# Kernel optimization log

Measured on AMD Instinct MI355X. Metric: run time of the kernel, lower is better.

## Reference

```python
import jax, jax.numpy as jnp
import numpy as np

TEMPERATURE = 0.1
NORMALIZED = True


def _l2norm(x, eps=1e-12):
    # matches F.normalize(p=2, dim=1)
    n = jnp.sqrt(jnp.sum(x * x, axis=1, keepdims=True))
    return x / jnp.maximum(n, eps)


def setup_inputs() -> dict:
    key = jax.random.key(0)
    k1, k2, k3, k4 = jax.random.split(key, 4)
    B, D = 4096, 256
    return {
        "hs": jax.random.normal(k1, (B, D), dtype=jnp.float32),
        "ht0": jax.random.normal(k2, (B, D), dtype=jnp.float32),
        "ht1": jax.random.normal(k3, (B, D), dtype=jnp.float32),
        "labels": jax.random.randint(k4, (B,), 0, 100, dtype=jnp.int64)
        if jax.config.jax_enable_x64 else jax.random.randint(k4, (B,), 0, 100, dtype=jnp.int32),
        "num_views": 2,
    }


def _per_teacher_loss(hs_n, ht_n, mask, logits_mask, batch_size, num_views):
    # features: [N, D] with N = 2B
    features = jnp.concatenate([hs_n, ht_n], axis=0)
    sim = jnp.matmul(features, features.T) / TEMPERATURE          # [N, N]
    exp_logits = jnp.exp(sim) * logits_mask                        # [N, N]
    log_prob = sim - jnp.log(jnp.sum(exp_logits, axis=1, keepdims=True))
    per_inst = -jnp.sum(mask * log_prob, axis=1) / jnp.sum(mask, axis=1)  # [N]
    if num_views > 1:
        per_inst = per_inst.reshape(batch_size, num_views).mean(axis=1)
    return per_inst.mean()


def reference(hs, ht0, ht1, labels, num_views):
    batch_size = labels.shape[0]
    hs = hs.reshape(batch_size, -1)
    ht_list = [ht0.reshape(batch_size, -1), ht1.reshape(batch_size, -1)]
    if NORMALIZED:
        hs = _l2norm(hs)
        ht_list = [_l2norm(ht) for ht in ht_list]

    labels2 = jnp.concatenate([labels, labels])                    # [N]
    mask = (labels2[:, None] == labels2[None, :]).astype(jnp.float32)
    N = 2 * batch_size
    logits_mask = 1.0 - jnp.eye(N, dtype=jnp.float32)              # zero diagonal
    mask = mask * logits_mask

    inter_loss = 0.0
    for ht in ht_list:
        inter_loss = inter_loss + _per_teacher_loss(
            hs, ht, mask, logits_mask, batch_size, num_views)
    return inter_loss / len(ht_list)
```

## Files before the change

### kernel.cpp

```cpp
#include <hip/hip_runtime.h>
#include <hip/hip_bf16.h>

#define B_SIZE 4096
#define D_SIZE 256
#define N_SIZE 8192
#define LOG2E10 14.4269504089f

#if __has_builtin(__builtin_amdgcn_exp2f)
#define FAST_EXP2(x) __builtin_amdgcn_exp2f(x)
#else
#define FAST_EXP2(x) __expf((x) * 0.69314718056f)
#endif

typedef __attribute__((ext_vector_type(8))) short short8;
typedef __attribute__((ext_vector_type(4))) short short4v;
typedef __attribute__((ext_vector_type(4))) float floatx4;


__device__ __forceinline__ void async16(void* lds, const void* g) {
    __builtin_amdgcn_global_load_lds(
        (const __attribute__((address_space(1))) unsigned int*)g,
        (__attribute__((address_space(3))) unsigned int*)lds, 16, 0, 0);
}

__device__ __forceinline__ void pair_from_q(int q, int& R, int& C) {
    int r = (int)((1.0f + sqrtf(1.0f + 8.0f * (float)q)) * 0.5f);
    while (r * (r - 1) / 2 > q) --r;
    while ((r + 1) * r / 2 <= q) ++r;
    R = r; C = q - r * (r - 1) / 2;
}

__global__ void norm_kernel(const float* __restrict__ hs,
                            const float* __restrict__ ht0,
                            const float* __restrict__ ht1,
                            __hip_bfloat16* __restrict__ dst,
                            float* __restrict__ zero_region,
                            const int* __restrict__ labels,
                            int* __restrict__ cnt, int* __restrict__ offv,
                            int* __restrict__ idxS) {
    const int tid = threadIdx.x;
    const int wv  = tid >> 6;
    const int l   = tid & 63;
    const int gid = blockIdx.x * 256 + tid;
    if (gid < 16386) zero_region[gid] = 0.0f;

    const int row = blockIdx.x * 4 + wv;
    const float* src = (row < 4096) ? (hs + row * D_SIZE)
                     : (row < 8192) ? (ht0 + (row - 4096) * D_SIZE)
                                    : (ht1 + (row - 8192) * D_SIZE);
    floatx4 x = *reinterpret_cast<const floatx4*>(src + l * 4);
    float ss = x[0] * x[0] + x[1] * x[1] + x[2] * x[2] + x[3] * x[3];
#pragma unroll
    for (int off = 32; off > 0; off >>= 1) ss += __shfl_xor(ss, off);
    float inv = 1.0f / fmaxf(sqrtf(ss), 1e-12f);
    short4v o;
#pragma unroll
    for (int k = 0; k < 4; ++k) {
        __hip_bfloat16 h = __float2bfloat16(x[k] * inv);
        o[k] = *reinterpret_cast<short*>(&h);
    }
    *reinterpret_cast<short4v*>(dst + row * D_SIZE + l * 4) = o;

    if (blockIdx.x == 0) {
        __shared__ int h[128], o2[128], ctr[128];
        if (tid < 128) { h[tid] = 0; ctr[tid] = 0; }
        __syncthreads();
        for (int i = tid; i < B_SIZE; i += 256) atomicAdd(&h[labels[i] & 127], 1);
        __syncthreads();
        if (tid == 0) {
            int s = 0;
            for (int c = 0; c < 128; ++c) { o2[c] = s; s += h[c]; }
        }
        __syncthreads();
        for (int i = tid; i < B_SIZE; i += 256) {
            int lab = labels[i] & 127;
            int pos = o2[lab] + atomicAdd(&ctr[lab], 1);
            idxS[pos] = i;
        }
        if (tid < 128) { cnt[tid] = h[tid]; offv[tid] = o2[tid]; }
    }
}

__global__ void gvec_kernel(const __hip_bfloat16* __restrict__ featBase,
                            const int* __restrict__ cnt,
                            const int* __restrict__ off,
                            const int* __restrict__ idxS,
                            float* __restrict__ gOut) {
    const int c   = blockIdx.x & 127;
    const int set = blockIdx.x >> 7;
    const int tid = threadIdx.x;
    const __hip_bfloat16* f = featBase + set * B_SIZE * D_SIZE;
    __shared__ int sIdx[256];
    const int n = cnt[c], o = off[c];
    float acc = 0.0f;
    for (int base = 0; base < n; base += 256) {
        int m = n - base; if (m > 256) m = 256;
        __syncthreads();
        if (tid < m) sIdx[tid] = idxS[o + base + tid];
        __syncthreads();
        for (int k = 0; k < m; ++k)
            acc += __bfloat162float(f[sIdx[k] * D_SIZE + tid]);
    }
    gOut[set * 32768 + c * 256 + tid] = acc;
}

__global__ __launch_bounds__(256, 2)
void sim_kernel(const __hip_bfloat16* __restrict__ featS,
                const __hip_bfloat16* __restrict__ featT0,
                const __hip_bfloat16* __restrict__ featT1,
                float* __restrict__ Sarr) {
    __shared__ __align__(16) unsigned char sB[2][32768];

    const int tid  = threadIdx.x;
    const int w    = tid >> 6;
    const int l    = tid & 63;
    const int quad = l >> 4;
    const int lcol = l & 15;

    int itemR[3], itemC[3], itemT[3], ni;
    if (blockIdx.x < 480) {
        ni = 2;
#pragma unroll
        for (int k = 0; k < 2; ++k) {
            int m = blockIdx.x * 2 + k;
            pair_from_q(m >> 1, itemR[k], itemC[k]);
            itemT[k] = m & 1;
        }
    } else {
        ni = 3;
        int i = blockIdx.x - 480;
        int m = 960 + i;
        pair_from_q(m >> 1, itemR[0], itemC[0]);
        itemT[0] = m & 1;
        itemR[1] = itemC[1] = i; itemT[1] = 0;
        itemR[2] = itemC[2] = i; itemT[2] = 1;
    }

    for (int it = 0; it < ni; ++it) {
        const int R = itemR[it], C = itemC[it], t = itemT[it];
        const __hip_bfloat16* featT = t ? featT1 : featT0;
        const int row_base = R * 256 + w * 64;
        const int col0 = C * 256;

        short8 af[4][8];
#pragma unroll
        for (int rt = 0; rt < 4; ++rt) {
            int arow = row_base + rt * 16 + lcol;
            const __hip_bfloat16* ap = (arow < B_SIZE) ? featS + arow * D_SIZE
                                                       : featT + (arow - B_SIZE) * D_SIZE;
#pragma unroll
            for (int ks = 0; ks < 8; ++ks)
                af[rt][ks] = *reinterpret_cast<const short8*>(ap + ks * 32 + quad * 8);
        }

        float Sp[4][4];
#pragma unroll
        for (int rt = 0; rt < 4; ++rt)
#pragma unroll
            for (int r = 0; r < 4; ++r) Sp[rt][r] = 0.0f;

        auto stage = [&](int b, int cb) {
            int tb = cb + w * 16;
            const __hip_bfloat16* cp = (tb < B_SIZE) ? featS + tb * D_SIZE
                                                     : featT + (tb - B_SIZE) * D_SIZE;
            const char* gp = (const char*)cp + (l & 15) * 512 + (l >> 4) * 16;
            unsigned char* lp = &sB[b][w * 8192];
#pragma unroll
            for (int ks = 0; ks < 8; ++ks)
                async16(lp + ks * 1024, gp + ks * 64);
        };

        stage(0, col0);

        for (int g = 0; g < 4; ++g) {
            const int buf = g & 1;
            __syncthreads();
            if (g + 1 < 4) stage(buf ^ 1, col0 + (g + 1) * 64);

            const int gcol = col0 + g * 64;
            if (gcol > row_base) continue;
            const bool dg = (gcol == row_base);

            float Cp[4] = {0.f, 0.f, 0.f, 0.f};
#pragma unroll
            for (int up = 0; up < 2; ++up) {
                floatx4 acc[2][4];
#pragma unroll
                for (int j = 0; j < 2; ++j)
#pragma unroll
                    for (int rt = 0; rt < 4; ++rt) acc[j][rt] = floatx4{0.f, 0.f, 0.f, 0.f};

#pragma unroll
                for (int ks = 0; ks < 8; ++ks) {
                    short8 bf[2];
#pragma unroll
                    for (int j = 0; j < 2; ++j)
                        bf[j] = *reinterpret_cast<const short8*>(
                            &sB[buf][(up * 2 + j) * 8192 + ks * 1024 + l * 16]);
#pragma unroll
                    for (int j = 0; j < 2; ++j)
#pragma unroll
                        for (int rt = 0; rt < 4; ++rt)
                            acc[j][rt] = __builtin_amdgcn_mfma_f32_16x16x32_bf16(
                                af[rt][ks], bf[j], acc[j][rt], 0, 0, 0);
                }
#pragma unroll
                for (int j = 0; j < 2; ++j)
#pragma unroll
                    for (int rt = 0; rt < 4; ++rt)
#pragma unroll
                        for (int r = 0; r < 4; ++r) {
                            float e = FAST_EXP2(acc[j][rt][r] * LOG2E10);
                            Sp[rt][r] += e;
                            Cp[up * 2 + j] += e;
                        }
            }

            if (!dg) {
#pragma unroll
                for (int u = 0; u < 4; ++u) {
                    Cp[u] += __shfl_xor(Cp[u], 16);
                    Cp[u] += __shfl_xor(Cp[u], 32);
                }
                if (quad == 0) {
#pragma unroll
                    for (int u = 0; u < 4; ++u)
                        atomicAdd(&Sarr[t * N_SIZE + gcol + u * 16 + lcol], Cp[u]);
                }
            }
        }

#pragma unroll
        for (int rt = 0; rt < 4; ++rt)
#pragma unroll
            for (int r = 0; r < 4; ++r) {
#pragma unroll
                for (int m = 1; m < 16; m <<= 1) Sp[rt][r] += __shfl_xor(Sp[rt][r], m);
            }
        if (lcol == 0) {
#pragma unroll
            for (int rt = 0; rt < 4; ++rt)
#pragma unroll
                for (int r = 0; r < 4; ++r) {
                    int row = row_base + rt * 16 + quad * 4 + r;
                    atomicAdd(&Sarr[t * N_SIZE + row], Sp[rt][r]);
                }
        }
    }
}

__global__ void rowstat_kernel(const __hip_bfloat16* __restrict__ featS,
                               const __hip_bfloat16* __restrict__ featT0,
                               const __hip_bfloat16* __restrict__ featT1,
                               const int* __restrict__ labels,
                               const float* __restrict__ gAll,
                               const int* __restrict__ cnt,
                               const float* __restrict__ Sarr,
                               float* __restrict__ lossAcc,
                               int* __restrict__ ticket,
                               float* __restrict__ out) {
    __shared__ float wpart[4];
    const int tid = threadIdx.x;
    const int wv  = tid >> 6;
    const int l   = tid & 63;
    const int waveid = blockIdx.x * 4 + wv;
    float psum = 0.0f;

    for (int it = 0; it < 8; ++it) {
        int R = waveid * 8 + it;
        int t = R >> 13;
        int i = R & (N_SIZE - 1);
        const __hip_bfloat16* f = (i < B_SIZE) ? featS + i * D_SIZE
                                : (t ? featT1 : featT0) + (i - B_SIZE) * D_SIZE;
        int lab = labels[i & (B_SIZE - 1)] & 127;
        short4v fb = *reinterpret_cast<const short4v*>(f + l * 4);
        float fx[4];
#pragma unroll
        for (int k = 0; k < 4; ++k) {
            unsigned int u = ((unsigned int)(unsigned short)fb[k]) << 16;
            fx[k] = __uint_as_float(u);
        }
        const float* gS = gAll + lab * 256 + l * 4;
        const float* gT = gAll + (1 + t) * 32768 + lab * 256 + l * 4;
        float dot = 0.f, aii = 0.f;
#pragma unroll
        for (int k = 0; k < 4; ++k) {
            dot += fx[k] * (gS[k] + gT[k]);
            aii += fx[k] * fx[k];
        }
#pragma unroll
        for (int m = 1; m < 64; m <<= 1) {
            dot += __shfl_xor(dot, m);
            aii += __shfl_xor(aii, m);
        }
        if (l == 0) {
            float S = Sarr[t * N_SIZE + i];
            float M = 2.0f * (float)cnt[lab] - 1.0f;
            float E = FAST_EXP2(LOG2E10 * aii);
            psum += logf(S - E) - 10.0f * (dot - aii) / M;
        }
    }
    if (l == 0) wpart[wv] = psum;
    __syncthreads();
    if (tid == 0) {
        atomicAdd(lossAcc, wpart[0] + wpart[1] + wpart[2] + wpart[3]);
        __threadfence();
        if (atomicAdd(ticket, 1) == 511) {
            float tot = atomicAdd(lossAcc, 0.0f);
            out[0] = tot / 16384.0f;
        }
    }
}

extern "C" void kernel_launch(void* const* d_in, const int* in_sizes, int n_in,
                              void* d_out, int out_size, void* d_ws, size_t ws_size,
                              hipStream_t stream) {
    const float* hs     = (const float*)d_in[0];
    const float* ht0    = (const float*)d_in[1];
    const float* ht1    = (const float*)d_in[2];
    const int*   labels = (const int*)d_in[3];

    char* ws = (char*)d_ws;
    float* Sarr    = (float*)(ws);
    float* lossAcc = (float*)(ws + 65536);
    int*   ticket  = (int*)(ws + 65540);
    int*   cnt     = (int*)(ws + 66048);
    int*   offv    = (int*)(ws + 66560);
    int*   idxS    = (int*)(ws + 67072);
    float* gAll    = (float*)(ws + 83968);
    __hip_bfloat16* featS  = (__hip_bfloat16*)(ws + 524288);
    __hip_bfloat16* featT0 = (__hip_bfloat16*)(ws + 524288 + 2097152);
    __hip_bfloat16* featT1 = (__hip_bfloat16*)(ws + 524288 + 2 * 2097152);

    norm_kernel<<<3072, 256, 0, stream>>>(hs, ht0, ht1, featS, (float*)ws,
                                          labels, cnt, offv, idxS);
    gvec_kernel<<<384, 256, 0, stream>>>(featS, cnt, offv, idxS, gAll);
    sim_kernel<<<512, 256, 0, stream>>>(featS, featT0, featT1, Sarr);
    rowstat_kernel<<<512, 256, 0, stream>>>(featS, featT0, featT1, labels, gAll, cnt,
                                            Sarr, lossAcc, ticket, (float*)d_out);
}
```

Baseline: 176.2 us.

## Use 512-row by 256-col sim tiles with single-shot LDS staging

The similarity kernel now runs 512-thread blocks (8 waves), each covering 512 rows against a 256-column strip. Each block loads the whole 256-column B tile into four LDS buffers in one async pass, replacing the double-buffered per-group pipeline and the multi-item loop. The triangular tile mapping is recomputed for the new 2:1 tile shape, with a separate path for diagonal blocks. The goal is more reuse of each LDS B tile across rows and fewer barriers, at the cost of 128KB of LDS per block, which limits occupancy, and no overlap between loads and compute.

```diff
diff --git a/kernel.cpp b/kernel.cpp
--- a/kernel.cpp
+++ b/kernel.cpp
@@ -21,13 +21,6 @@
     __builtin_amdgcn_global_load_lds(
         (const __attribute__((address_space(1))) unsigned int*)g,
         (__attribute__((address_space(3))) unsigned int*)lds, 16, 0, 0);
-}
-
-__device__ __forceinline__ void pair_from_q(int q, int& R, int& C) {
-    int r = (int)((1.0f + sqrtf(1.0f + 8.0f * (float)q)) * 0.5f);
-    while (r * (r - 1) / 2 > q) --r;
-    while ((r + 1) * r / 2 <= q) ++r;
-    R = r; C = q - r * (r - 1) / 2;
 }
 
 __global__ void norm_kernel(const float* __restrict__ hs,
@@ -104,12 +97,12 @@
     gOut[set * 32768 + c * 256 + tid] = acc;
 }
 
-__global__ __launch_bounds__(256, 2)
+__global__ __launch_bounds__(512, 2)
 void sim_kernel(const __hip_bfloat16* __restrict__ featS,
                 const __hip_bfloat16* __restrict__ featT0,
                 const __hip_bfloat16* __restrict__ featT1,
                 float* __restrict__ Sarr) {
-    __shared__ __align__(16) unsigned char sB[2][32768];
+    __shared__ __align__(16) unsigned char sB[4][32768];
 
     const int tid  = threadIdx.x;
     const int w    = tid >> 6;
@@ -117,135 +110,130 @@
     const int quad = l >> 4;
     const int lcol = l & 15;
 
-    int itemR[3], itemC[3], itemT[3], ni;
+    int RB, C, t;
     if (blockIdx.x < 480) {
-        ni = 2;
-#pragma unroll
-        for (int k = 0; k < 2; ++k) {
-            int m = blockIdx.x * 2 + k;
-            pair_from_q(m >> 1, itemR[k], itemC[k]);
-            itemT[k] = m & 1;
-        }
+        t = blockIdx.x & 1;
+        int q = blockIdx.x >> 1;
+        int r = (int)((1.0f + sqrtf(1.0f + 4.0f * (float)q)) * 0.5f);
+        while (r * (r - 1) > q) --r;
+        while (r * (r + 1) <= q) ++r;
+        RB = r; C = q - r * (r - 1);
     } else {
-        ni = 3;
         int i = blockIdx.x - 480;
-        int m = 960 + i;
-        pair_from_q(m >> 1, itemR[0], itemC[0]);
-        itemT[0] = m & 1;
-        itemR[1] = itemC[1] = i; itemT[1] = 0;
-        itemR[2] = itemC[2] = i; itemT[2] = 1;
-    }
-
-    for (int it = 0; it < ni; ++it) {
-        const int R = itemR[it], C = itemC[it], t = itemT[it];
-        const __hip_bfloat16* featT = t ? featT1 : featT0;
-        const int row_base = R * 256 + w * 64;
-        const int col0 = C * 256;
-
-        short8 af[4][8];
-#pragma unroll
-        for (int rt = 0; rt < 4; ++rt) {
-            int arow = row_base + rt * 16 + lcol;
-            const __hip_bfloat16* ap = (arow < B_SIZE) ? featS + arow * D_SIZE
-                                                       : featT + (arow - B_SIZE) * D_SIZE;
-#pragma unroll
-            for (int ks = 0; ks < 8; ++ks)
-                af[rt][ks] = *reinterpret_cast<const short8*>(ap + ks * 32 + quad * 8);
-        }
-
-        float Sp[4][4];
+        t = i & 1;
+        int s = i >> 1;
+        RB = s >> 1;
+        C = (RB << 1) + (s & 1);
+    }
+
+    const __hip_bfloat16* featT = t ? featT1 : featT0;
+    const int row_base = RB * 512 + w * 64;
+    const int col0 = C * 256;
+
+    short8 af[4][8];
+#pragma unroll
+    for (int rt = 0; rt < 4; ++rt) {
+        int arow = row_base + rt * 16 + lcol;
+        const __hip_bfloat16* ap = (arow < B_SIZE) ? featS + arow * D_SIZE
+                                                   : featT + (arow - B_SIZE) * D_SIZE;
+#pragma unroll
+        for (int ks = 0; ks < 8; ++ks)
+            af[rt][ks] = *reinterpret_cast<const short8*>(ap + ks * 32 + quad * 8);
+    }
+
+    {
+        const int u   = w >> 1;
+        const int ks0 = (w & 1) * 4;
+        const int tb  = col0 + u * 16;
+        const __hip_bfloat16* cp = (tb < B_SIZE) ? featS + tb * D_SIZE
+                                                 : featT + (tb - B_SIZE) * D_SIZE;
+        const char* gp = (const char*)cp + (l & 15) * 512 + (l >> 4) * 16;
+#pragma unroll
+        for (int g = 0; g < 4; ++g)
+#pragma unroll
+            for (int kk = 0; kk < 4; ++kk) {
+                int ks = ks0 + kk;
+                async16(&sB[g][u * 8192 + ks * 1024], gp + g * 32768 + ks * 64);
+            }
+    }
+
+    float Sp[4][4];
+#pragma unroll
+    for (int rt = 0; rt < 4; ++rt)
+#pragma unroll
+        for (int r = 0; r < 4; ++r) Sp[rt][r] = 0.0f;
+
+    __syncthreads();
+
+    for (int g = 0; g < 4; ++g) {
+        const int gcol = col0 + g * 64;
+        if (gcol > row_base) continue;
+        const bool dg = (gcol == row_base);
+
+        float Cp[4] = {0.f, 0.f, 0.f, 0.f};
+#pragma unroll
+        for (int up = 0; up < 2; ++up) {
+            floatx4 acc[2][4];
+#pragma unroll
+            for (int j = 0; j < 2; ++j)
+#pragma unroll
+                for (int rt = 0; rt < 4; ++rt) acc[j][rt] = floatx4{0.f, 0.f, 0.f, 0.f};
+
+#pragma unroll
+            for (int ks = 0; ks < 8; ++ks) {
+                short8 bf[2];
+#pragma unroll
+                for (int j = 0; j < 2; ++j)
+                    bf[j] = *reinterpret_cast<const short8*>(
+                        &sB[g][(up * 2 + j) * 8192 + ks * 1024 + l * 16]);
+#pragma unroll
+                for (int j = 0; j < 2; ++j)
+#pragma unroll
+                    for (int rt = 0; rt < 4; ++rt)
+                        acc[j][rt] = __builtin_amdgcn_mfma_f32_16x16x32_bf16(
+                            af[rt][ks], bf[j], acc[j][rt], 0, 0, 0);
+            }
+#pragma unroll
+            for (int j = 0; j < 2; ++j)
+#pragma unroll
+                for (int rt = 0; rt < 4; ++rt)
+#pragma unroll
+                    for (int r = 0; r < 4; ++r) {
+                        float e = FAST_EXP2(acc[j][rt][r] * LOG2E10);
+                        Sp[rt][r] += e;
+                        Cp[up * 2 + j] += e;
+                    }
+        }
+
+        if (!dg) {
+#pragma unroll
+            for (int u = 0; u < 4; ++u) {
+                Cp[u] += __shfl_xor(Cp[u], 16);
+                Cp[u] += __shfl_xor(Cp[u], 32);
+            }
+            if (quad == 0) {
+#pragma unroll
+                for (int u = 0; u < 4; ++u)
+                    atomicAdd(&Sarr[t * N_SIZE + gcol + u * 16 + lcol], Cp[u]);
+            }
+        }
+    }
+
+#pragma unroll
+    for (int rt = 0; rt < 4; ++rt)
+#pragma unroll
+        for (int r = 0; r < 4; ++r) {
+#pragma unroll
+            for (int m = 1; m < 16; m <<= 1) Sp[rt][r] += __shfl_xor(Sp[rt][r], m);
+        }
+    if (lcol == 0) {
 #pragma unroll
         for (int rt = 0; rt < 4; ++rt)
 #pragma unroll
-            for (int r = 0; r < 4; ++r) Sp[rt][r] = 0.0f;
-
-        auto stage = [&](int b, int cb) {
-            int tb = cb + w * 16;
-            const __hip_bfloat16* cp = (tb < B_SIZE) ? featS + tb * D_SIZE
-                                                     : featT + (tb - B_SIZE) * D_SIZE;
-            const char* gp = (const char*)cp + (l & 15) * 512 + (l >> 4) * 16;
-            unsigned char* lp = &sB[b][w * 8192];
-#pragma unroll
-            for (int ks = 0; ks < 8; ++ks)
-                async16(lp + ks * 1024, gp + ks * 64);
-        };
-
-        stage(0, col0);
-
-        for (int g = 0; g < 4; ++g) {
-            const int buf = g & 1;
-            __syncthreads();
-            if (g + 1 < 4) stage(buf ^ 1, col0 + (g + 1) * 64);
-
-            const int gcol = col0 + g * 64;
-            if (gcol > row_base) continue;
-            const bool dg = (gcol == row_base);
-
-            float Cp[4] = {0.f, 0.f, 0.f, 0.f};
-#pragma unroll
-            for (int up = 0; up < 2; ++up) {
-                floatx4 acc[2][4];
-#pragma unroll
-                for (int j = 0; j < 2; ++j)
-#pragma unroll
-                    for (int rt = 0; rt < 4; ++rt) acc[j][rt] = floatx4{0.f, 0.f, 0.f, 0.f};
-
-#pragma unroll
-                for (int ks = 0; ks < 8; ++ks) {
-                    short8 bf[2];
-#pragma unroll
-                    for (int j = 0; j < 2; ++j)
-                        bf[j] = *reinterpret_cast<const short8*>(
-                            &sB[buf][(up * 2 + j) * 8192 + ks * 1024 + l * 16]);
-#pragma unroll
-                    for (int j = 0; j < 2; ++j)
-#pragma unroll
-                        for (int rt = 0; rt < 4; ++rt)
-                            acc[j][rt] = __builtin_amdgcn_mfma_f32_16x16x32_bf16(
-                                af[rt][ks], bf[j], acc[j][rt], 0, 0, 0);
-                }
-#pragma unroll
-                for (int j = 0; j < 2; ++j)
-#pragma unroll
-                    for (int rt = 0; rt < 4; ++rt)
-#pragma unroll
-                        for (int r = 0; r < 4; ++r) {
-                            float e = FAST_EXP2(acc[j][rt][r] * LOG2E10);
-                            Sp[rt][r] += e;
-                            Cp[up * 2 + j] += e;
-                        }
-            }
-
-            if (!dg) {
-#pragma unroll
-                for (int u = 0; u < 4; ++u) {
-                    Cp[u] += __shfl_xor(Cp[u], 16);
-                    Cp[u] += __shfl_xor(Cp[u], 32);
-                }
-                if (quad == 0) {
-#pragma unroll
-                    for (int u = 0; u < 4; ++u)
-                        atomicAdd(&Sarr[t * N_SIZE + gcol + u * 16 + lcol], Cp[u]);
-                }
-            }
-        }
-
-#pragma unroll
-        for (int rt = 0; rt < 4; ++rt)
-#pragma unroll
             for (int r = 0; r < 4; ++r) {
-#pragma unroll
-                for (int m = 1; m < 16; m <<= 1) Sp[rt][r] += __shfl_xor(Sp[rt][r], m);
-            }
-        if (lcol == 0) {
-#pragma unroll
-            for (int rt = 0; rt < 4; ++rt)
-#pragma unroll
-                for (int r = 0; r < 4; ++r) {
-                    int row = row_base + rt * 16 + quad * 4 + r;
-                    atomicAdd(&Sarr[t * N_SIZE + row], Sp[rt][r]);
-                }
-        }
+                int row = row_base + rt * 16 + quad * 4 + r;
+                atomicAdd(&Sarr[t * N_SIZE + row], Sp[rt][r]);
+            }
     }
 }
 
@@ -335,7 +323,7 @@
     norm_kernel<<<3072, 256, 0, stream>>>(hs, ht0, ht1, featS, (float*)ws,
                                           labels, cnt, offv, idxS);
     gvec_kernel<<<384, 256, 0, stream>>>(featS, cnt, offv, idxS, gAll);
-    sim_kernel<<<512, 256, 0, stream>>>(featS, featT0, featT1, Sarr);
+    sim_kernel<<<544, 512, 0, stream>>>(featS, featT0, featT1, Sarr);
     rowstat_kernel<<<512, 256, 0, stream>>>(featS, featT0, featT1, labels, gAll, cnt,
                                             Sarr, lossAcc, ticket, (float*)d_out);
 }
```

Result: no change. 177.0 us (+0.4%).

## Fuse label grouping and class sums into per-class loss kernel, simplify sim grid

Applied to the files above, without the earlier changes.

The label histogram and sort in the norm kernel, plus the separate gvec kernel, are removed. They are replaced by a classstat kernel that launches one block per class: each block gathers its member indices, builds the class feature sums in shared memory, and computes the per-instance loss terms. The sim kernel drops its hand-balanced 2-or-3 tiles per block and launches a 528x2 grid with one triangular tile per block, the diagonal now included in the pair indexing. This cuts one launch and the global gather buffers, but loses the sim load balancing. Per-class blocks also make the final loss stage uneven and only 128 blocks wide.

```diff
diff --git a/kernel.cpp b/kernel.cpp
--- a/kernel.cpp
+++ b/kernel.cpp
@@ -9,7 +9,7 @@
 #if __has_builtin(__builtin_amdgcn_exp2f)
 #define FAST_EXP2(x) __builtin_amdgcn_exp2f(x)
 #else
-#define FAST_EXP2(x) __expf((x) * 0.69314718056f)
+#define FAST_EXP2(x) exp2f(x)
 #endif
 
 typedef __attribute__((ext_vector_type(8))) short short8;
@@ -25,19 +25,16 @@
 
 __device__ __forceinline__ void pair_from_q(int q, int& R, int& C) {
     int r = (int)((1.0f + sqrtf(1.0f + 8.0f * (float)q)) * 0.5f);
-    while (r * (r - 1) / 2 > q) --r;
-    while ((r + 1) * r / 2 <= q) ++r;
-    R = r; C = q - r * (r - 1) / 2;
+    while (r * (r + 1) / 2 > q) --r;
+    while ((r + 1) * (r + 2) / 2 <= q) ++r;
+    R = r; C = q - r * (r + 1) / 2;
 }
 
 __global__ void norm_kernel(const float* __restrict__ hs,
                             const float* __restrict__ ht0,
                             const float* __restrict__ ht1,
                             __hip_bfloat16* __restrict__ dst,
-                            float* __restrict__ zero_region,
-                            const int* __restrict__ labels,
-                            int* __restrict__ cnt, int* __restrict__ offv,
-                            int* __restrict__ idxS) {
+                            float* __restrict__ zero_region) {
     const int tid = threadIdx.x;
     const int wv  = tid >> 6;
     const int l   = tid & 63;
@@ -60,48 +57,6 @@
         o[k] = *reinterpret_cast<short*>(&h);
     }
     *reinterpret_cast<short4v*>(dst + row * D_SIZE + l * 4) = o;
-
-    if (blockIdx.x == 0) {
-        __shared__ int h[128], o2[128], ctr[128];
-        if (tid < 128) { h[tid] = 0; ctr[tid] = 0; }
-        __syncthreads();
-        for (int i = tid; i < B_SIZE; i += 256) atomicAdd(&h[labels[i] & 127], 1);
-        __syncthreads();
-        if (tid == 0) {
-            int s = 0;
-            for (int c = 0; c < 128; ++c) { o2[c] = s; s += h[c]; }
-        }
-        __syncthreads();
-        for (int i = tid; i < B_SIZE; i += 256) {
-            int lab = labels[i] & 127;
-            int pos = o2[lab] + atomicAdd(&ctr[lab], 1);
-            idxS[pos] = i;
-        }
-        if (tid < 128) { cnt[tid] = h[tid]; offv[tid] = o2[tid]; }
-    }
-}
-
-__global__ void gvec_kernel(const __hip_bfloat16* __restrict__ featBase,
-                            const int* __restrict__ cnt,
-                            const int* __restrict__ off,
-                            const int* __restrict__ idxS,
-                            float* __restrict__ gOut) {
-    const int c   = blockIdx.x & 127;
-    const int set = blockIdx.x >> 7;
-    const int tid = threadIdx.x;
-    const __hip_bfloat16* f = featBase + set * B_SIZE * D_SIZE;
-    __shared__ int sIdx[256];
-    const int n = cnt[c], o = off[c];
-    float acc = 0.0f;
-    for (int base = 0; base < n; base += 256) {
-        int m = n - base; if (m > 256) m = 256;
-        __syncthreads();
-        if (tid < m) sIdx[tid] = idxS[o + base + tid];
-        __syncthreads();
-        for (int k = 0; k < m; ++k)
-            acc += __bfloat162float(f[sIdx[k] * D_SIZE + tid]);
-    }
-    gOut[set * 32768 + c * 256 + tid] = acc;
 }
 
 __global__ __launch_bounds__(256, 2)
@@ -111,182 +66,182 @@
                 float* __restrict__ Sarr) {
     __shared__ __align__(16) unsigned char sB[2][32768];
 
+    const int p = blockIdx.x;
+    const int t = blockIdx.y;
+    const __hip_bfloat16* featT = t ? featT1 : featT0;
+
+    int R, C;
+    pair_from_q(p, R, C);
+
     const int tid  = threadIdx.x;
     const int w    = tid >> 6;
     const int l    = tid & 63;
     const int quad = l >> 4;
     const int lcol = l & 15;
-
-    int itemR[3], itemC[3], itemT[3], ni;
-    if (blockIdx.x < 480) {
-        ni = 2;
-#pragma unroll
-        for (int k = 0; k < 2; ++k) {
-            int m = blockIdx.x * 2 + k;
-            pair_from_q(m >> 1, itemR[k], itemC[k]);
-            itemT[k] = m & 1;
-        }
-    } else {
-        ni = 3;
-        int i = blockIdx.x - 480;
-        int m = 960 + i;
-        pair_from_q(m >> 1, itemR[0], itemC[0]);
-        itemT[0] = m & 1;
-        itemR[1] = itemC[1] = i; itemT[1] = 0;
-        itemR[2] = itemC[2] = i; itemT[2] = 1;
-    }
-
-    for (int it = 0; it < ni; ++it) {
-        const int R = itemR[it], C = itemC[it], t = itemT[it];
-        const __hip_bfloat16* featT = t ? featT1 : featT0;
-        const int row_base = R * 256 + w * 64;
-        const int col0 = C * 256;
-
-        short8 af[4][8];
-#pragma unroll
-        for (int rt = 0; rt < 4; ++rt) {
-            int arow = row_base + rt * 16 + lcol;
-            const __hip_bfloat16* ap = (arow < B_SIZE) ? featS + arow * D_SIZE
-                                                       : featT + (arow - B_SIZE) * D_SIZE;
-#pragma unroll
-            for (int ks = 0; ks < 8; ++ks)
-                af[rt][ks] = *reinterpret_cast<const short8*>(ap + ks * 32 + quad * 8);
-        }
-
-        float Sp[4][4];
+    const int row_base = R * 256 + w * 64;
+
+    short8 af[4][8];
+#pragma unroll
+    for (int rt = 0; rt < 4; ++rt) {
+        int arow = row_base + rt * 16 + lcol;
+        const __hip_bfloat16* ap = (arow < B_SIZE) ? featS + arow * D_SIZE
+                                                   : featT + (arow - B_SIZE) * D_SIZE;
+#pragma unroll
+        for (int ks = 0; ks < 8; ++ks)
+            af[rt][ks] = *reinterpret_cast<const short8*>(ap + ks * 32 + quad * 8);
+    }
+
+    float Sp[4][4];
+#pragma unroll
+    for (int rt = 0; rt < 4; ++rt)
+#pragma unroll
+        for (int r = 0; r < 4; ++r) Sp[rt][r] = 0.0f;
+
+    const int col0 = C * 256;
+
+    auto stage = [&](int b, int cb) {
+        int tb = cb + w * 16;
+        const __hip_bfloat16* cp = (tb < B_SIZE) ? featS + tb * D_SIZE
+                                                 : featT + (tb - B_SIZE) * D_SIZE;
+        const char* gp = (const char*)cp + (l & 15) * 512 + (l >> 4) * 16;
+        unsigned char* lp = &sB[b][w * 8192];
+#pragma unroll
+        for (int ks = 0; ks < 8; ++ks)
+            async16(lp + ks * 1024, gp + ks * 64);
+    };
+
+    stage(0, col0);
+
+    for (int g = 0; g < 4; ++g) {
+        const int buf = g & 1;
+        __syncthreads();
+        if (g + 1 < 4) stage(buf ^ 1, col0 + (g + 1) * 64);
+
+        const int gcol = col0 + g * 64;
+        if (gcol > row_base) continue;
+        const bool dg = (gcol == row_base);
+
+        float Cp[4] = {0.f, 0.f, 0.f, 0.f};
+#pragma unroll
+        for (int up = 0; up < 2; ++up) {
+            floatx4 acc[2][4];
+#pragma unroll
+            for (int j = 0; j < 2; ++j)
+#pragma unroll
+                for (int rt = 0; rt < 4; ++rt) acc[j][rt] = floatx4{0.f, 0.f, 0.f, 0.f};
+
+#pragma unroll
+            for (int ks = 0; ks < 8; ++ks) {
+                short8 bf[2];
+#pragma unroll
+                for (int j = 0; j < 2; ++j)
+                    bf[j] = *reinterpret_cast<const short8*>(
+                        &sB[buf][(up * 2 + j) * 8192 + ks * 1024 + l * 16]);
+#pragma unroll
+                for (int j = 0; j < 2; ++j)
+#pragma unroll
+                    for (int rt = 0; rt < 4; ++rt)
+                        acc[j][rt] = __builtin_amdgcn_mfma_f32_16x16x32_bf16(
+                            af[rt][ks], bf[j], acc[j][rt], 0, 0, 0);
+            }
+#pragma unroll
+            for (int j = 0; j < 2; ++j)
+#pragma unroll
+                for (int rt = 0; rt < 4; ++rt)
+#pragma unroll
+                    for (int r = 0; r < 4; ++r) {
+                        float e = FAST_EXP2(acc[j][rt][r] * LOG2E10);
+                        Sp[rt][r] += e;
+                        Cp[up * 2 + j] += e;
+                    }
+        }
+
+        if (!dg) {
+#pragma unroll
+            for (int u = 0; u < 4; ++u) {
+                Cp[u] += __shfl_xor(Cp[u], 16);
+                Cp[u] += __shfl_xor(Cp[u], 32);
+            }
+            if (quad == 0) {
+#pragma unroll
+                for (int u = 0; u < 4; ++u)
+                    atomicAdd(&Sarr[t * N_SIZE + gcol + u * 16 + lcol], Cp[u]);
+            }
+        }
+    }
+
+#pragma unroll
+    for (int rt = 0; rt < 4; ++rt)
+#pragma unroll
+        for (int r = 0; r < 4; ++r) {
+#pragma unroll
+            for (int m = 1; m < 16; m <<= 1) Sp[rt][r] += __shfl_xor(Sp[rt][r], m);
+        }
+    if (lcol == 0) {
 #pragma unroll
         for (int rt = 0; rt < 4; ++rt)
 #pragma unroll
-            for (int r = 0; r < 4; ++r) Sp[rt][r] = 0.0f;
-
-        auto stage = [&](int b, int cb) {
-            int tb = cb + w * 16;
-            const __hip_bfloat16* cp = (tb < B_SIZE) ? featS + tb * D_SIZE
-                                                     : featT + (tb - B_SIZE) * D_SIZE;
-            const char* gp = (const char*)cp + (l & 15) * 512 + (l >> 4) * 16;
-            unsigned char* lp = &sB[b][w * 8192];
-#pragma unroll
-            for (int ks = 0; ks < 8; ++ks)
-                async16(lp + ks * 1024, gp + ks * 64);
-        };
-
-        stage(0, col0);
-
-        for (int g = 0; g < 4; ++g) {
-            const int buf = g & 1;
-            __syncthreads();
-            if (g + 1 < 4) stage(buf ^ 1, col0 + (g + 1) * 64);
-
-            const int gcol = col0 + g * 64;
-            if (gcol > row_base) continue;
-            const bool dg = (gcol == row_base);
-
-            float Cp[4] = {0.f, 0.f, 0.f, 0.f};
-#pragma unroll
-            for (int up = 0; up < 2; ++up) {
-                floatx4 acc[2][4];
-#pragma unroll
-                for (int j = 0; j < 2; ++j)
-#pragma unroll
-                    for (int rt = 0; rt < 4; ++rt) acc[j][rt] = floatx4{0.f, 0.f, 0.f, 0.f};
-
-#pragma unroll
-                for (int ks = 0; ks < 8; ++ks) {
-                    short8 bf[2];
-#pragma unroll
-                    for (int j = 0; j < 2; ++j)
-                        bf[j] = *reinterpret_cast<const short8*>(
-                            &sB[buf][(up * 2 + j) * 8192 + ks * 1024 + l * 16]);
-#pragma unroll
-                    for (int j = 0; j < 2; ++j)
-#pragma unroll
-                        for (int rt = 0; rt < 4; ++rt)
-                            acc[j][rt] = __builtin_amdgcn_mfma_f32_16x16x32_bf16(
-                                af[rt][ks], bf[j], acc[j][rt], 0, 0, 0);
-                }
-#pragma unroll
-                for (int j = 0; j < 2; ++j)
-#pragma unroll
-                    for (int rt = 0; rt < 4; ++rt)
-#pragma unroll
-                        for (int r = 0; r < 4; ++r) {
-                            float e = FAST_EXP2(acc[j][rt][r] * LOG2E10);
-                            Sp[rt][r] += e;
-                            Cp[up * 2 + j] += e;
-                        }
-            }
-
-            if (!dg) {
-#pragma unroll
-                for (int u = 0; u < 4; ++u) {
-                    Cp[u] += __shfl_xor(Cp[u], 16);
-                    Cp[u] += __shfl_xor(Cp[u], 32);
-                }
-                if (quad == 0) {
-#pragma unroll
-                    for (int u = 0; u < 4; ++u)
-                        atomicAdd(&Sarr[t * N_SIZE + gcol + u * 16 + lcol], Cp[u]);
-                }
-            }
-        }
-
-#pragma unroll
-        for (int rt = 0; rt < 4; ++rt)
-#pragma unroll
             for (int r = 0; r < 4; ++r) {
-#pragma unroll
-                for (int m = 1; m < 16; m <<= 1) Sp[rt][r] += __shfl_xor(Sp[rt][r], m);
-            }
-        if (lcol == 0) {
-#pragma unroll
-            for (int rt = 0; rt < 4; ++rt)
-#pragma unroll
-                for (int r = 0; r < 4; ++r) {
-                    int row = row_base + rt * 16 + quad * 4 + r;
-                    atomicAdd(&Sarr[t * N_SIZE + row], Sp[rt][r]);
-                }
-        }
-    }
-}
-
-__global__ void rowstat_kernel(const __hip_bfloat16* __restrict__ featS,
-                               const __hip_bfloat16* __restrict__ featT0,
-                               const __hip_bfloat16* __restrict__ featT1,
-                               const int* __restrict__ labels,
-                               const float* __restrict__ gAll,
-                               const int* __restrict__ cnt,
-                               const float* __restrict__ Sarr,
-                               float* __restrict__ lossAcc,
-                               int* __restrict__ ticket,
-                               float* __restrict__ out) {
+                int row = row_base + rt * 16 + quad * 4 + r;
+                atomicAdd(&Sarr[t * N_SIZE + row], Sp[rt][r]);
+            }
+    }
+}
+
+__global__ void classstat_kernel(const __hip_bfloat16* __restrict__ featS,
+                                 const __hip_bfloat16* __restrict__ featT0,
+                                 const __hip_bfloat16* __restrict__ featT1,
+                                 const int* __restrict__ labels,
+                                 const float* __restrict__ Sarr,
+                                 float* __restrict__ lossAcc,
+                                 int* __restrict__ ticket,
+                                 float* __restrict__ out) {
+    __shared__ int idx[256];
+    __shared__ int nsh;
+    __shared__ float gS[256], gT0[256], gT1[256];
     __shared__ float wpart[4];
+
+    const int c   = blockIdx.x;
     const int tid = threadIdx.x;
     const int wv  = tid >> 6;
     const int l   = tid & 63;
-    const int waveid = blockIdx.x * 4 + wv;
+
+    if (tid == 0) nsh = 0;
+    __syncthreads();
+    for (int i = tid; i < B_SIZE; i += 256)
+        if ((labels[i] & 127) == c) { int p = atomicAdd(&nsh, 1); idx[p] = i; }
+    __syncthreads();
+    const int n = nsh;
+
+    if (n > 0) {
+        float aS = 0.f, a0 = 0.f, a1 = 0.f;
+        for (int m = 0; m < n; ++m) {
+            int r = idx[m] * D_SIZE + tid;
+            aS += __bfloat162float(featS[r]);
+            a0 += __bfloat162float(featT0[r]);
+            a1 += __bfloat162float(featT1[r]);
+        }
+        gS[tid] = aS; gT0[tid] = a0; gT1[tid] = a1;
+    }
+    __syncthreads();
+
     float psum = 0.0f;
-
-    for (int it = 0; it < 8; ++it) {
-        int R = waveid * 8 + it;
-        int t = R >> 13;
-        int i = R & (N_SIZE - 1);
-        const __hip_bfloat16* f = (i < B_SIZE) ? featS + i * D_SIZE
-                                : (t ? featT1 : featT0) + (i - B_SIZE) * D_SIZE;
-        int lab = labels[i & (B_SIZE - 1)] & 127;
+    const float M = 2.0f * (float)n - 1.0f;
+    for (int inst = wv; inst < 4 * n; inst += 4) {
+        const int t    = inst & 1;
+        const int half = (inst >> 1) & 1;
+        const int i    = idx[inst >> 2];
+        const __hip_bfloat16* f = half ? ((t ? featT1 : featT0) + i * D_SIZE)
+                                       : (featS + i * D_SIZE);
         short4v fb = *reinterpret_cast<const short4v*>(f + l * 4);
-        float fx[4];
+        const float* gT = t ? gT1 : gT0;
+        float dot = 0.f, aii = 0.f;
 #pragma unroll
         for (int k = 0; k < 4; ++k) {
             unsigned int u = ((unsigned int)(unsigned short)fb[k]) << 16;
-            fx[k] = __uint_as_float(u);
-        }
-        const float* gS = gAll + lab * 256 + l * 4;
-        const float* gT = gAll + (1 + t) * 32768 + lab * 256 + l * 4;
-        float dot = 0.f, aii = 0.f;
-#pragma unroll
-        for (int k = 0; k < 4; ++k) {
-            dot += fx[k] * (gS[k] + gT[k]);
-            aii += fx[k] * fx[k];
+            float fx = __uint_as_float(u);
+            dot += fx * (gS[l * 4 + k] + gT[l * 4 + k]);
+            aii += fx * fx;
         }
 #pragma unroll
         for (int m = 1; m < 64; m <<= 1) {
@@ -294,8 +249,8 @@
             aii += __shfl_xor(aii, m);
         }
         if (l == 0) {
-            float S = Sarr[t * N_SIZE + i];
-            float M = 2.0f * (float)cnt[lab] - 1.0f;
+            int row = half ? (B_SIZE + i) : i;
+            float S = Sarr[t * N_SIZE + row];
             float E = FAST_EXP2(LOG2E10 * aii);
             psum += logf(S - E) - 10.0f * (dot - aii) / M;
         }
@@ -305,7 +260,7 @@
     if (tid == 0) {
         atomicAdd(lossAcc, wpart[0] + wpart[1] + wpart[2] + wpart[3]);
         __threadfence();
-        if (atomicAdd(ticket, 1) == 511) {
+        if (atomicAdd(ticket, 1) == 127) {
             float tot = atomicAdd(lossAcc, 0.0f);
             out[0] = tot / 16384.0f;
         }
@@ -324,18 +279,12 @@
     float* Sarr    = (float*)(ws);
     float* lossAcc = (float*)(ws + 65536);
     int*   ticket  = (int*)(ws + 65540);
-    int*   cnt     = (int*)(ws + 66048);
-    int*   offv    = (int*)(ws + 66560);
-    int*   idxS    = (int*)(ws + 67072);
-    float* gAll    = (float*)(ws + 83968);
     __hip_bfloat16* featS  = (__hip_bfloat16*)(ws + 524288);
     __hip_bfloat16* featT0 = (__hip_bfloat16*)(ws + 524288 + 2097152);
     __hip_bfloat16* featT1 = (__hip_bfloat16*)(ws + 524288 + 2 * 2097152);
 
-    norm_kernel<<<3072, 256, 0, stream>>>(hs, ht0, ht1, featS, (float*)ws,
-                                          labels, cnt, offv, idxS);
-    gvec_kernel<<<384, 256, 0, stream>>>(featS, cnt, offv, idxS, gAll);
-    sim_kernel<<<512, 256, 0, stream>>>(featS, featT0, featT1, Sarr);
-    rowstat_kernel<<<512, 256, 0, stream>>>(featS, featT0, featT1, labels, gAll, cnt,
-                                            Sarr, lossAcc, ticket, (float*)d_out);
-}
+    norm_kernel<<<3072, 256, 0, stream>>>(hs, ht0, ht1, featS, (float*)ws);
+    sim_kernel<<<dim3(528, 2), 256, 0, stream>>>(featS, featT0, featT1, Sarr);
+    classstat_kernel<<<128, 256, 0, stream>>>(featS, featT0, featT1, labels,
+                                              Sarr, lossAcc, ticket, (float*)d_out);
+}
```

Measured after the change: 167.2 us. 1.05x faster.
